# Optimization experiments

Measured on AMD Instinct MI355X. Metric: run time of the kernel, lower is better.

The kernel has to match this reference:

```python
import jax, jax.numpy as jnp
import numpy as np

Z_DIM = 64
K = 2048
N = 32768


def setup_inputs() -> dict:
    key = jax.random.key(0)
    k1, k2 = jax.random.split(key)
    x = jax.random.normal(k1, (N, Z_DIM), dtype=jnp.float32)
    # init.normal_(locs, std=sqrt(z_dim))
    locs = jax.random.normal(k2, (K, Z_DIM), dtype=jnp.float32) * np.sqrt(Z_DIM)
    logits = jnp.zeros((K,), dtype=jnp.float32)  # maxent buffer
    return {"x": x, "locs": locs, "logits": logits}


def reference(x, locs, logits):
    d = x.shape[-1]
    var = jnp.float32(d)  # scale = sqrt(z_dim) -> variance = z_dim
    # squared distances [N, K] via cdist expansion (avoids [N,K,d] intermediate)
    sq = (
        jnp.sum(x * x, axis=-1, keepdims=True)
        + jnp.sum(locs * locs, axis=-1)[None, :]
        - 2.0 * (x @ locs.T)
    )
    # Independent Normal log prob summed over z_dim
    log_norm_const = d * (0.5 * jnp.log(2.0 * jnp.pi) + 0.5 * jnp.log(var))
    comp_log_prob = -0.5 * sq / var - log_norm_const  # [N, K]
    mix_logits = jax.nn.log_softmax(logits)  # Categorical normalizes logits
    wlp = comp_log_prob + mix_logits  # weighted_log_prob, [N, K]
    log_prob = jax.nn.logsumexp(wlp, axis=-1)  # [N]
    modes = jnp.argmax(wlp, axis=-1)  # assign_modes, [N]
    quantized = locs[modes]  # hard_quantize, [N, z_dim]
    return log_prob, quantized
```

## Files before the change

### kernel.cpp

```cpp
#include <hip/hip_runtime.h>
#include <math.h>

#define N_SAMP 32768
#define K_COMP 2048
#define ZD 64
#define LNC 191.896324792608546f
#define LN2F 0.69314718055994531f
#define INV_LN2 1.44269504088896340f
#define S2C 0.02254211001388974f

#define TILES_TOT 128
#define KG 4
#define TILES (TILES_TOT / KG)

typedef __attribute__((ext_vector_type(8))) short short8;
typedef __attribute__((ext_vector_type(4))) float v4f;

#if __has_builtin(__builtin_amdgcn_exp2f)
#define EXP2(x) __builtin_amdgcn_exp2f(x)
#else
#define EXP2(x) exp2f(x)
#endif

__device__ inline unsigned short f2bf(float f) {
    unsigned int u = __float_as_uint(f);
    u += 0x7fffu + ((u >> 16) & 1u);
    return (unsigned short)(u >> 16);
}
__device__ inline float bf2f(unsigned short h) {
    return __uint_as_float(((unsigned int)h) << 16);
}

__global__ __launch_bounds__(256) void prep_kernel(
    const float* __restrict__ locs, const float* __restrict__ logits,
    float* __restrict__ ck2, float* __restrict__ lse_out,
    char* __restrict__ lf) {
    if (blockIdx.x < 32) {
        int gid = blockIdx.x * 256 + threadIdx.x;
        int T = gid >> 6;
        int l = gid & 63;
        int n = l & 15, q = l >> 4;
        int k = T * 16 + n;

        const float* src = locs + (size_t)k * ZD + q * 8;
        float4 u0 = *(const float4*)(src);
        float4 u1 = *(const float4*)(src + 4);
        float4 u2 = *(const float4*)(src + 32);
        float4 u3 = *(const float4*)(src + 36);
        float a[8] = {u0.x, u0.y, u0.z, u0.w, u1.x, u1.y, u1.z, u1.w};
        float b[8] = {u2.x, u2.y, u2.z, u2.w, u3.x, u3.y, u3.z, u3.w};

        short8 h0, h1, l0, l1;
        float sq = 0.f;
#pragma unroll
        for (int j = 0; j < 8; ++j) {
            unsigned short ha = f2bf(a[j]);
            h0[j] = (short)ha; l0[j] = (short)f2bf(a[j] - bf2f(ha));
            unsigned short hb = f2bf(b[j]);
            h1[j] = (short)hb; l1[j] = (short)f2bf(b[j] - bf2f(hb));
            sq = fmaf(a[j], a[j], sq);
            sq = fmaf(b[j], b[j], sq);
        }
        char* dst = lf + (size_t)T * 4096 + l * 16;
        *(short8*)(dst)        = h0;
        *(short8*)(dst + 1024) = h1;
        *(short8*)(dst + 2048) = l0;
        *(short8*)(dst + 3072) = l1;

        sq += __shfl_xor(sq, 16);
        sq += __shfl_xor(sq, 32);
        if (q == 0) ck2[k] = (logits[k] - sq * (1.0f / 128.0f)) * INV_LN2;
    } else {
        __shared__ float red[4];
        int tid = threadIdx.x;
        int wv = tid >> 6, ln = tid & 63;
        float lm = -INFINITY;
        for (int i = tid; i < K_COMP; i += 256) lm = fmaxf(lm, logits[i]);
#pragma unroll
        for (int d = 1; d < 64; d <<= 1) lm = fmaxf(lm, __shfl_xor(lm, d));
        if (ln == 0) red[wv] = lm;
        __syncthreads();
        float M = fmaxf(fmaxf(red[0], red[1]), fmaxf(red[2], red[3]));
        float ls = 0.f;
        for (int i = tid; i < K_COMP; i += 256) ls += __expf(logits[i] - M);
#pragma unroll
        for (int d = 1; d < 64; d <<= 1) ls += __shfl_xor(ls, d);
        __syncthreads();
        if (ln == 0) red[wv] = ls;
        __syncthreads();
        if (tid == 0) *lse_out = M + __logf(red[0] + red[1] + red[2] + red[3]);
    }
}

__global__ __launch_bounds__(512, 4) void mix_kernel(
    const float* __restrict__ x, const float* __restrict__ locs,
    const char* __restrict__ lf, const float* __restrict__ ck2,
    const float* __restrict__ lse_ptr, float* __restrict__ out) {

    __shared__ float sm[KG][2][32];
    __shared__ float ss[KG][2][32];
    __shared__ int   sa[KG][2][32];
    __shared__ float xsq_sh[64];
    __shared__ int   amax_sh[64];

    const int tid  = threadIdx.x;
    const int lane = tid & 63;
    const int wave = tid >> 6;
    const int kg   = __builtin_amdgcn_readfirstlane(wave & 3);
    const int sgp  = __builtin_amdgcn_readfirstlane(wave >> 2);
    const int n    = lane & 15;
    const int quad = lane >> 4;
    const int sA   = blockIdx.x * 64 + sgp * 32 + n;
    const int sB   = sA + 16;

    short8 bhA0, bhA1, blA0, blA1, bhB0, bhB1, blB0, blB1;
    {
        const float* xp = x + (size_t)sA * ZD + quad * 8;
        float4 u0 = *(const float4*)(xp);
        float4 u1 = *(const float4*)(xp + 4);
        float4 u2 = *(const float4*)(xp + 32);
        float4 u3 = *(const float4*)(xp + 36);
        const float* yp = x + (size_t)sB * ZD + quad * 8;
        float4 v0 = *(const float4*)(yp);
        float4 v1 = *(const float4*)(yp + 4);
        float4 v2 = *(const float4*)(yp + 32);
        float4 v3 = *(const float4*)(yp + 36);
        float a[8] = {u0.x, u0.y, u0.z, u0.w, u1.x, u1.y, u1.z, u1.w};
        float b[8] = {u2.x, u2.y, u2.z, u2.w, u3.x, u3.y, u3.z, u3.w};
        float c[8] = {v0.x, v0.y, v0.z, v0.w, v1.x, v1.y, v1.z, v1.w};
        float d[8] = {v2.x, v2.y, v2.z, v2.w, v3.x, v3.y, v3.z, v3.w};
        float pa = 0.f, pb = 0.f;
#pragma unroll
        for (int j = 0; j < 8; ++j) {
            unsigned short h;
            h = f2bf(a[j]); bhA0[j] = (short)h; blA0[j] = (short)f2bf(a[j] - bf2f(h));
            h = f2bf(b[j]); bhA1[j] = (short)h; blA1[j] = (short)f2bf(b[j] - bf2f(h));
            h = f2bf(c[j]); bhB0[j] = (short)h; blB0[j] = (short)f2bf(c[j] - bf2f(h));
            h = f2bf(d[j]); bhB1[j] = (short)h; blB1[j] = (short)f2bf(d[j] - bf2f(h));
            pa = fmaf(a[j], a[j], pa); pa = fmaf(b[j], b[j], pa);
            pb = fmaf(c[j], c[j], pb); pb = fmaf(d[j], d[j], pb);
        }
        pa += __shfl_xor(pa, 16); pa += __shfl_xor(pa, 32);
        pb += __shfl_xor(pb, 16); pb += __shfl_xor(pb, 32);
        if (kg == 0) {
            if (quad == 0) xsq_sh[sgp * 32 + n] = pa;
            if (quad == 1) xsq_sh[sgp * 32 + 16 + n] = pb;
        }
    }

    const char* aw = lf + (size_t)kg * TILES * 4096 + lane * 16;
    const float* ckw = ck2 + kg * TILES * 16 + quad * 4;
    const int kb0 = kg * TILES * 16 + quad * 4;

    short8 fa[2][4];
    float4 fc[2];

#define LOADA(slot, tt) do {                                     \
    const char* _p = aw + (size_t)(tt) * 4096;                   \
    fa[slot][0] = *(const short8*)(_p);                          \
    fa[slot][1] = *(const short8*)(_p + 1024);                   \
    fa[slot][2] = *(const short8*)(_p + 2048);                   \
    fa[slot][3] = *(const short8*)(_p + 3072);                   \
    fc[slot] = *(const float4*)(ckw + (tt) * 16);                \
} while (0)

    float mA = -1e30f, mB = -1e30f;
    float sA0 = 0.f, sA1 = 0.f, sB0 = 0.f, sB1 = 0.f;
    int aiA = 0, aiB = 0;

#define COMPUTE(slot, tt) do {                                                 \
    v4f accA = {0.f, 0.f, 0.f, 0.f};                                           \
    v4f accB = {0.f, 0.f, 0.f, 0.f};                                           \
    accA = __builtin_amdgcn_mfma_f32_16x16x32_bf16(fa[slot][0], bhA0, accA, 0, 0, 0); \
    accB = __builtin_amdgcn_mfma_f32_16x16x32_bf16(fa[slot][0], bhB0, accB, 0, 0, 0); \
    accA = __builtin_amdgcn_mfma_f32_16x16x32_bf16(fa[slot][1], bhA1, accA, 0, 0, 0); \
    accB = __builtin_amdgcn_mfma_f32_16x16x32_bf16(fa[slot][1], bhB1, accB, 0, 0, 0); \
    accA = __builtin_amdgcn_mfma_f32_16x16x32_bf16(fa[slot][0], blA0, accA, 0, 0, 0); \
    accB = __builtin_amdgcn_mfma_f32_16x16x32_bf16(fa[slot][0], blB0, accB, 0, 0, 0); \
    accA = __builtin_amdgcn_mfma_f32_16x16x32_bf16(fa[slot][1], blA1, accA, 0, 0, 0); \
    accB = __builtin_amdgcn_mfma_f32_16x16x32_bf16(fa[slot][1], blB1, accB, 0, 0, 0); \
    accA = __builtin_amdgcn_mfma_f32_16x16x32_bf16(fa[slot][2], bhA0, accA, 0, 0, 0); \
    accB = __builtin_amdgcn_mfma_f32_16x16x32_bf16(fa[slot][2], bhB0, accB, 0, 0, 0); \
    accA = __builtin_amdgcn_mfma_f32_16x16x32_bf16(fa[slot][3], bhA1, accA, 0, 0, 0); \
    accB = __builtin_amdgcn_mfma_f32_16x16x32_bf16(fa[slot][3], bhB1, accB, 0, 0, 0); \
    const int kb = kb0 + (tt) * 16;                                            \
    float4 cc = fc[slot];                                                      \
    {                                                                          \
        float w0 = fmaf(accA.x, S2C, cc.x);                                    \
        float w1 = fmaf(accA.y, S2C, cc.y);                                    \
        float w2 = fmaf(accA.z, S2C, cc.z);                                    \
        float w3 = fmaf(accA.w, S2C, cc.w);                                    \
        sA0 += EXP2(w0) + EXP2(w1);                                            \
        sA1 += EXP2(w2) + EXP2(w3);                                            \
        float t01 = fmaxf(w0, w1); int i01 = (w1 > w0) ? (kb + 1) : (kb + 0);  \
        float t23 = fmaxf(w2, w3); int i23 = (w3 > w2) ? (kb + 3) : (kb + 2);  \
        float tt2 = fmaxf(t01, t23); int it = (t23 > t01) ? i23 : i01;         \
        aiA = (tt2 > mA) ? it : aiA; mA = fmaxf(mA, tt2);                      \
    }                                                                          \
    {                                                                          \
        float w0 = fmaf(accB.x, S2C, cc.x);                                    \
        float w1 = fmaf(accB.y, S2C, cc.y);                                    \
        float w2 = fmaf(accB.z, S2C, cc.z);                                    \
        float w3 = fmaf(accB.w, S2C, cc.w);                                    \
        sB0 += EXP2(w0) + EXP2(w1);                                            \
        sB1 += EXP2(w2) + EXP2(w3);                                            \
        float t01 = fmaxf(w0, w1); int i01 = (w1 > w0) ? (kb + 1) : (kb + 0);  \
        float t23 = fmaxf(w2, w3); int i23 = (w3 > w2) ? (kb + 3) : (kb + 2);  \
        float tt2 = fmaxf(t01, t23); int it = (t23 > t01) ? i23 : i01;         \
        aiB = (tt2 > mB) ? it : aiB; mB = fmaxf(mB, tt2);                      \
    }                                                                          \
} while (0)

    LOADA(0, 0);
    for (int t = 0; t < TILES; t += 2) {
        int t1 = (t + 1 < TILES) ? (t + 1) : (TILES - 1);
        LOADA(1, t1);
        COMPUTE(0, t);
        int t2 = (t + 2 < TILES) ? (t + 2) : (TILES - 1);
        LOADA(0, t2);
        COMPUTE(1, t + 1);
    }

    float sumA = sA0 + sA1;
    float sumB = sB0 + sB1;

#pragma unroll
    for (int d = 16; d <= 32; d <<= 1) {
        sumA += __shfl_xor(sumA, d);
        sumB += __shfl_xor(sumB, d);
        float om; int oa;
        om = __shfl_xor(mA, d); oa = __shfl_xor(aiA, d);
        aiA = (om > mA || (om == mA && oa < aiA)) ? oa : aiA;
        mA = fmaxf(mA, om);
        om = __shfl_xor(mB, d); oa = __shfl_xor(aiB, d);
        aiB = (om > mB || (om == mB && oa < aiB)) ? oa : aiB;
        mB = fmaxf(mB, om);
    }
    if (quad == 0) { sm[kg][sgp][n] = mA; ss[kg][sgp][n] = sumA; sa[kg][sgp][n] = aiA; }
    if (quad == 1) { sm[kg][sgp][16 + n] = mB; ss[kg][sgp][16 + n] = sumB; sa[kg][sgp][16 + n] = aiB; }
    __syncthreads();

    if (tid < 64) {
        int g = tid >> 5, sl = tid & 31;
        float M = -1e30f, S = 0.f; int A = 0;
#pragma unroll
        for (int k = 0; k < KG; ++k) {
            float mw = sm[k][g][sl];
            int aw2 = sa[k][g][sl];
            S += ss[k][g][sl];
            A = (mw > M || (mw == M && aw2 < A)) ? aw2 : A;
            M = fmaxf(M, mw);
        }
        float bias = -xsq_sh[tid] * (1.0f / 128.0f) - LNC;
        out[blockIdx.x * 64 + tid] = fmaf(__log2f(S), LN2F, bias - lse_ptr[0]);
        amax_sh[tid] = A;
    }
    __syncthreads();

    const float4* lq = (const float4*)locs;
    float4* oq = (float4*)(out + N_SAMP + (size_t)blockIdx.x * 64 * ZD);
#pragma unroll
    for (int i = tid; i < 64 * (ZD / 4); i += 512) {
        int r = i >> 4, c = i & 15;
        oq[i] = lq[(size_t)amax_sh[r] * (ZD / 4) + c];
    }
#undef LOADA
#undef COMPUTE
}

extern "C" void kernel_launch(void* const* d_in, const int* in_sizes, int n_in,
                              void* d_out, int out_size, void* d_ws, size_t ws_size,
                              hipStream_t stream) {
    const float* x      = (const float*)d_in[0];
    const float* locs   = (const float*)d_in[1];
    const float* logits = (const float*)d_in[2];
    float* out = (float*)d_out;

    float* ck2 = (float*)d_ws;
    float* lse = ck2 + K_COMP;
    char*  lf  = (char*)d_ws + 16384;

    prep_kernel<<<33, 256, 0, stream>>>(locs, logits, ck2, lse, lf);
    mix_kernel<<<N_SAMP / 64, 512, 0, stream>>>(x, locs, lf, ck2, lse, out);
}
```

Baseline: 97.14 us.

## Have each wave process four sample tiles to reuse locs fragments

The block shrinks from eight waves to four. Each wave now covers all 64 samples of the block as four 16-row tiles for its quarter of the components, instead of two tiles. Each locs fragment loaded from global memory therefore feeds twice as many MFMAs, which halves locs fragment traffic per block and gives the matrix units more independent accumulators to interleave. The cost is more VGPRs per wave (the x fragments and per-tile reduction state are four-wide), the launch-bound occupancy hint drops, and there are fewer waves per block to hide latency.

Result: no change. 95.51 us (-1.7%).

```diff
diff --git a/kernel.cpp b/kernel.cpp
--- a/kernel.cpp
+++ b/kernel.cpp
@@ -9,9 +9,8 @@
 #define INV_LN2 1.44269504088896340f
 #define S2C 0.02254211001388974f
 
-#define TILES_TOT 128
 #define KG 4
-#define TILES (TILES_TOT / KG)
+#define TILES (K_COMP / 16 / KG)
 
 typedef __attribute__((ext_vector_type(8))) short short8;
 typedef __attribute__((ext_vector_type(4))) float v4f;
@@ -92,60 +91,46 @@
     }
 }
 
-__global__ __launch_bounds__(512, 4) void mix_kernel(
+__global__ __launch_bounds__(256, 2) void mix_kernel(
     const float* __restrict__ x, const float* __restrict__ locs,
     const char* __restrict__ lf, const float* __restrict__ ck2,
     const float* __restrict__ lse_ptr, float* __restrict__ out) {
 
-    __shared__ float sm[KG][2][32];
-    __shared__ float ss[KG][2][32];
-    __shared__ int   sa[KG][2][32];
-    __shared__ float xsq_sh[64];
+    __shared__ float sm[KG][64];
+    __shared__ float ss[KG][64];
+    __shared__ int   sa[KG][64];
     __shared__ int   amax_sh[64];
 
     const int tid  = threadIdx.x;
     const int lane = tid & 63;
-    const int wave = tid >> 6;
-    const int kg   = __builtin_amdgcn_readfirstlane(wave & 3);
-    const int sgp  = __builtin_amdgcn_readfirstlane(wave >> 2);
+    const int kg   = __builtin_amdgcn_readfirstlane(tid >> 6);
     const int n    = lane & 15;
     const int quad = lane >> 4;
-    const int sA   = blockIdx.x * 64 + sgp * 32 + n;
-    const int sB   = sA + 16;
-
-    short8 bhA0, bhA1, blA0, blA1, bhB0, bhB1, blB0, blB1;
-    {
-        const float* xp = x + (size_t)sA * ZD + quad * 8;
+    const int sbase = blockIdx.x * 64;
+
+    short8 bh[4][2], bl[4][2];
+    float xs[4];
+#pragma unroll
+    for (int bt = 0; bt < 4; ++bt) {
+        const float* xp = x + (size_t)(sbase + bt * 16 + n) * ZD + quad * 8;
         float4 u0 = *(const float4*)(xp);
         float4 u1 = *(const float4*)(xp + 4);
         float4 u2 = *(const float4*)(xp + 32);
         float4 u3 = *(const float4*)(xp + 36);
-        const float* yp = x + (size_t)sB * ZD + quad * 8;
-        float4 v0 = *(const float4*)(yp);
-        float4 v1 = *(const float4*)(yp + 4);
-        float4 v2 = *(const float4*)(yp + 32);
-        float4 v3 = *(const float4*)(yp + 36);
         float a[8] = {u0.x, u0.y, u0.z, u0.w, u1.x, u1.y, u1.z, u1.w};
         float b[8] = {u2.x, u2.y, u2.z, u2.w, u3.x, u3.y, u3.z, u3.w};
-        float c[8] = {v0.x, v0.y, v0.z, v0.w, v1.x, v1.y, v1.z, v1.w};
-        float d[8] = {v2.x, v2.y, v2.z, v2.w, v3.x, v3.y, v3.z, v3.w};
-        float pa = 0.f, pb = 0.f;
+        float p = 0.f;
 #pragma unroll
         for (int j = 0; j < 8; ++j) {
             unsigned short h;
-            h = f2bf(a[j]); bhA0[j] = (short)h; blA0[j] = (short)f2bf(a[j] - bf2f(h));
-            h = f2bf(b[j]); bhA1[j] = (short)h; blA1[j] = (short)f2bf(b[j] - bf2f(h));
-            h = f2bf(c[j]); bhB0[j] = (short)h; blB0[j] = (short)f2bf(c[j] - bf2f(h));
-            h = f2bf(d[j]); bhB1[j] = (short)h; blB1[j] = (short)f2bf(d[j] - bf2f(h));
-            pa = fmaf(a[j], a[j], pa); pa = fmaf(b[j], b[j], pa);
-            pb = fmaf(c[j], c[j], pb); pb = fmaf(d[j], d[j], pb);
-        }
-        pa += __shfl_xor(pa, 16); pa += __shfl_xor(pa, 32);
-        pb += __shfl_xor(pb, 16); pb += __shfl_xor(pb, 32);
-        if (kg == 0) {
-            if (quad == 0) xsq_sh[sgp * 32 + n] = pa;
-            if (quad == 1) xsq_sh[sgp * 32 + 16 + n] = pb;
-        }
+            h = f2bf(a[j]); bh[bt][0][j] = (short)h; bl[bt][0][j] = (short)f2bf(a[j] - bf2f(h));
+            h = f2bf(b[j]); bh[bt][1][j] = (short)h; bl[bt][1][j] = (short)f2bf(b[j] - bf2f(h));
+            p = fmaf(a[j], a[j], p);
+            p = fmaf(b[j], b[j], p);
+        }
+        p += __shfl_xor(p, 16);
+        p += __shfl_xor(p, 32);
+        xs[bt] = p;
     }
 
     const char* aw = lf + (size_t)kg * TILES * 4096 + lane * 16;
@@ -164,51 +149,52 @@
     fc[slot] = *(const float4*)(ckw + (tt) * 16);                \
 } while (0)
 
-    float mA = -1e30f, mB = -1e30f;
-    float sA0 = 0.f, sA1 = 0.f, sB0 = 0.f, sB1 = 0.f;
-    int aiA = 0, aiB = 0;
-
-#define COMPUTE(slot, tt) do {                                                 \
-    v4f accA = {0.f, 0.f, 0.f, 0.f};                                           \
-    v4f accB = {0.f, 0.f, 0.f, 0.f};                                           \
-    accA = __builtin_amdgcn_mfma_f32_16x16x32_bf16(fa[slot][0], bhA0, accA, 0, 0, 0); \
-    accB = __builtin_amdgcn_mfma_f32_16x16x32_bf16(fa[slot][0], bhB0, accB, 0, 0, 0); \
-    accA = __builtin_amdgcn_mfma_f32_16x16x32_bf16(fa[slot][1], bhA1, accA, 0, 0, 0); \
-    accB = __builtin_amdgcn_mfma_f32_16x16x32_bf16(fa[slot][1], bhB1, accB, 0, 0, 0); \
-    accA = __builtin_amdgcn_mfma_f32_16x16x32_bf16(fa[slot][0], blA0, accA, 0, 0, 0); \
-    accB = __builtin_amdgcn_mfma_f32_16x16x32_bf16(fa[slot][0], blB0, accB, 0, 0, 0); \
-    accA = __builtin_amdgcn_mfma_f32_16x16x32_bf16(fa[slot][1], blA1, accA, 0, 0, 0); \
-    accB = __builtin_amdgcn_mfma_f32_16x16x32_bf16(fa[slot][1], blB1, accB, 0, 0, 0); \
-    accA = __builtin_amdgcn_mfma_f32_16x16x32_bf16(fa[slot][2], bhA0, accA, 0, 0, 0); \
-    accB = __builtin_amdgcn_mfma_f32_16x16x32_bf16(fa[slot][2], bhB0, accB, 0, 0, 0); \
-    accA = __builtin_amdgcn_mfma_f32_16x16x32_bf16(fa[slot][3], bhA1, accA, 0, 0, 0); \
-    accB = __builtin_amdgcn_mfma_f32_16x16x32_bf16(fa[slot][3], bhB1, accB, 0, 0, 0); \
-    const int kb = kb0 + (tt) * 16;                                            \
-    float4 cc = fc[slot];                                                      \
-    {                                                                          \
-        float w0 = fmaf(accA.x, S2C, cc.x);                                    \
-        float w1 = fmaf(accA.y, S2C, cc.y);                                    \
-        float w2 = fmaf(accA.z, S2C, cc.z);                                    \
-        float w3 = fmaf(accA.w, S2C, cc.w);                                    \
-        sA0 += EXP2(w0) + EXP2(w1);                                            \
-        sA1 += EXP2(w2) + EXP2(w3);                                            \
-        float t01 = fmaxf(w0, w1); int i01 = (w1 > w0) ? (kb + 1) : (kb + 0);  \
-        float t23 = fmaxf(w2, w3); int i23 = (w3 > w2) ? (kb + 3) : (kb + 2);  \
-        float tt2 = fmaxf(t01, t23); int it = (t23 > t01) ? i23 : i01;         \
-        aiA = (tt2 > mA) ? it : aiA; mA = fmaxf(mA, tt2);                      \
-    }                                                                          \
-    {                                                                          \
-        float w0 = fmaf(accB.x, S2C, cc.x);                                    \
-        float w1 = fmaf(accB.y, S2C, cc.y);                                    \
-        float w2 = fmaf(accB.z, S2C, cc.z);                                    \
-        float w3 = fmaf(accB.w, S2C, cc.w);                                    \
-        sB0 += EXP2(w0) + EXP2(w1);                                            \
-        sB1 += EXP2(w2) + EXP2(w3);                                            \
-        float t01 = fmaxf(w0, w1); int i01 = (w1 > w0) ? (kb + 1) : (kb + 0);  \
-        float t23 = fmaxf(w2, w3); int i23 = (w3 > w2) ? (kb + 3) : (kb + 2);  \
-        float tt2 = fmaxf(t01, t23); int it = (t23 > t01) ? i23 : i01;         \
-        aiB = (tt2 > mB) ? it : aiB; mB = fmaxf(mB, tt2);                      \
-    }                                                                          \
+    float mm[4] = {-1e30f, -1e30f, -1e30f, -1e30f};
+    float s0[4] = {0.f, 0.f, 0.f, 0.f};
+    float s1[4] = {0.f, 0.f, 0.f, 0.f};
+    int   ai[4] = {0, 0, 0, 0};
+
+#define COMPUTE(slot, tt) do {                                                  \
+    v4f acc[4];                                                                 \
+    _Pragma("unroll")                                                           \
+    for (int bt = 0; bt < 4; ++bt) acc[bt] = (v4f){0.f, 0.f, 0.f, 0.f};         \
+    _Pragma("unroll")                                                           \
+    for (int h = 0; h < 2; ++h) {                                               \
+        _Pragma("unroll")                                                       \
+        for (int bt = 0; bt < 4; ++bt)                                          \
+            acc[bt] = __builtin_amdgcn_mfma_f32_16x16x32_bf16(                  \
+                fa[slot][h], bh[bt][h], acc[bt], 0, 0, 0);                      \
+    }                                                                           \
+    _Pragma("unroll")                                                           \
+    for (int h = 0; h < 2; ++h) {                                               \
+        _Pragma("unroll")                                                       \
+        for (int bt = 0; bt < 4; ++bt)                                          \
+            acc[bt] = __builtin_amdgcn_mfma_f32_16x16x32_bf16(                  \
+                fa[slot][h], bl[bt][h], acc[bt], 0, 0, 0);                      \
+    }                                                                           \
+    _Pragma("unroll")                                                           \
+    for (int h = 0; h < 2; ++h) {                                               \
+        _Pragma("unroll")                                                       \
+        for (int bt = 0; bt < 4; ++bt)                                          \
+            acc[bt] = __builtin_amdgcn_mfma_f32_16x16x32_bf16(                  \
+                fa[slot][2 + h], bh[bt][h], acc[bt], 0, 0, 0);                  \
+    }                                                                           \
+    const int kb = kb0 + (tt) * 16;                                             \
+    float4 cc = fc[slot];                                                       \
+    _Pragma("unroll")                                                           \
+    for (int bt = 0; bt < 4; ++bt) {                                            \
+        float w0 = fmaf(acc[bt].x, S2C, cc.x);                                  \
+        float w1 = fmaf(acc[bt].y, S2C, cc.y);                                  \
+        float w2 = fmaf(acc[bt].z, S2C, cc.z);                                  \
+        float w3 = fmaf(acc[bt].w, S2C, cc.w);                                  \
+        s0[bt] += EXP2(w0) + EXP2(w1);                                          \
+        s1[bt] += EXP2(w2) + EXP2(w3);                                          \
+        float t01 = fmaxf(w0, w1); int i01 = (w1 > w0) ? (kb + 1) : (kb + 0);   \
+        float t23 = fmaxf(w2, w3); int i23 = (w3 > w2) ? (kb + 3) : (kb + 2);   \
+        float tt2 = fmaxf(t01, t23); int it = (t23 > t01) ? i23 : i01;          \
+        ai[bt] = (tt2 > mm[bt]) ? it : ai[bt];                                  \
+        mm[bt] = fmaxf(mm[bt], tt2);                                            \
+    }                                                                           \
 } while (0)
 
     LOADA(0, 0);
@@ -221,46 +207,48 @@
         COMPUTE(1, t + 1);
     }
 
-    float sumA = sA0 + sA1;
-    float sumB = sB0 + sB1;
-
-#pragma unroll
-    for (int d = 16; d <= 32; d <<= 1) {
-        sumA += __shfl_xor(sumA, d);
-        sumB += __shfl_xor(sumB, d);
-        float om; int oa;
-        om = __shfl_xor(mA, d); oa = __shfl_xor(aiA, d);
-        aiA = (om > mA || (om == mA && oa < aiA)) ? oa : aiA;
-        mA = fmaxf(mA, om);
-        om = __shfl_xor(mB, d); oa = __shfl_xor(aiB, d);
-        aiB = (om > mB || (om == mB && oa < aiB)) ? oa : aiB;
-        mB = fmaxf(mB, om);
-    }
-    if (quad == 0) { sm[kg][sgp][n] = mA; ss[kg][sgp][n] = sumA; sa[kg][sgp][n] = aiA; }
-    if (quad == 1) { sm[kg][sgp][16 + n] = mB; ss[kg][sgp][16 + n] = sumB; sa[kg][sgp][16 + n] = aiB; }
+#pragma unroll
+    for (int bt = 0; bt < 4; ++bt) {
+        float sum = s0[bt] + s1[bt];
+#pragma unroll
+        for (int d = 16; d <= 32; d <<= 1) {
+            sum += __shfl_xor(sum, d);
+            float om = __shfl_xor(mm[bt], d);
+            int   oa = __shfl_xor(ai[bt], d);
+            ai[bt] = (om > mm[bt] || (om == mm[bt] && oa < ai[bt])) ? oa : ai[bt];
+            mm[bt] = fmaxf(mm[bt], om);
+        }
+        if (quad == 0) {
+            sm[kg][bt * 16 + n] = mm[bt];
+            ss[kg][bt * 16 + n] = sum;
+            sa[kg][bt * 16 + n] = ai[bt];
+        }
+    }
     __syncthreads();
 
     if (tid < 64) {
-        int g = tid >> 5, sl = tid & 31;
-        float M = -1e30f, S = 0.f; int A = 0;
+        float M = -1e30f, S = 0.f;
+        int A = 0;
 #pragma unroll
         for (int k = 0; k < KG; ++k) {
-            float mw = sm[k][g][sl];
-            int aw2 = sa[k][g][sl];
-            S += ss[k][g][sl];
+            float mw = sm[k][tid];
+            int aw2 = sa[k][tid];
+            S += ss[k][tid];
             A = (mw > M || (mw == M && aw2 < A)) ? aw2 : A;
             M = fmaxf(M, mw);
         }
-        float bias = -xsq_sh[tid] * (1.0f / 128.0f) - LNC;
-        out[blockIdx.x * 64 + tid] = fmaf(__log2f(S), LN2F, bias - lse_ptr[0]);
+        float myxs = (quad == 0) ? xs[0] : (quad == 1) ? xs[1]
+                   : (quad == 2) ? xs[2] : xs[3];
+        float bias = -myxs * (1.0f / 128.0f) - LNC;
+        out[sbase + tid] = fmaf(__log2f(S), LN2F, bias - lse_ptr[0]);
         amax_sh[tid] = A;
     }
     __syncthreads();
 
     const float4* lq = (const float4*)locs;
-    float4* oq = (float4*)(out + N_SAMP + (size_t)blockIdx.x * 64 * ZD);
-#pragma unroll
-    for (int i = tid; i < 64 * (ZD / 4); i += 512) {
+    float4* oq = (float4*)(out + N_SAMP + (size_t)sbase * ZD);
+#pragma unroll
+    for (int i = tid; i < 64 * (ZD / 4); i += 256) {
         int r = i >> 4, c = i & 15;
         oq[i] = lq[(size_t)amax_sh[r] * (ZD / 4) + c];
     }
@@ -281,5 +269,5 @@
     char*  lf  = (char*)d_ws + 16384;
 
     prep_kernel<<<33, 256, 0, stream>>>(locs, logits, ck2, lse, lf);
-    mix_kernel<<<N_SAMP / 64, 512, 0, stream>>>(x, locs, lf, ck2, lse, out);
-}
+    mix_kernel<<<N_SAMP / 64, 256, 0, stream>>>(x, locs, lf, ck2, lse, out);
+}
```
